# Kernel optimization log

Measured on AMD Instinct MI355X. Metric: run time of the kernel, lower is better.

The kernel has to match this reference:

```python
import jax, jax.numpy as jnp
import numpy as np

B, N, C = 32, 1025, 768
H, D = 12, 64          # num_heads, head_dim
M = 4 * D              # num random features = 256
HEIGHT, WIDTH = 32, 32 # spatial grid; N = HEIGHT*WIDTH + 1 (CLS)
EPS = 1e-6


def setup_inputs() -> dict:
    key = jax.random.key(0)
    ks = jax.random.split(key, 7)
    x = jax.random.normal(ks[0], (B, N, C), jnp.float32)
    w_qkv = jax.random.normal(ks[1], (3 * C, C), jnp.float32) * 0.02
    w_proj = jax.random.normal(ks[2], (C, C), jnp.float32) * 0.02
    b_proj = jnp.zeros((C,), jnp.float32)
    c_row = jax.random.normal(ks[3], (H, D), jnp.float32) * 0.02
    c_col = jax.random.normal(ks[4], (H, D), jnp.float32) * 0.02
    # orthogonal random-feature projection (m, d): QR blocks scaled by chi norm
    blocks = []
    for i in range(M // D):
        Hm = jax.random.normal(jax.random.fold_in(ks[5], i), (D, D), jnp.float32)
        Q, _ = jnp.linalg.qr(Hm)
        nrm = jnp.linalg.norm(jax.random.normal(jax.random.fold_in(ks[6], i), (D,), jnp.float32))
        blocks.append(Q * nrm)
    proj_feat = jnp.concatenate(blocks, axis=0)  # (M, D)
    return {"x": x, "w_qkv": w_qkv, "w_proj": w_proj, "b_proj": b_proj,
            "c_row": c_row, "c_col": c_col, "proj_feat": proj_feat}


def _string(xp, c_row, c_col):
    """Circulant-STRING rotation. xp: (B,H,Np,D)."""
    rows = jnp.arange(HEIGHT, dtype=jnp.float32)
    cols = jnp.arange(WIDTH, dtype=jnp.float32)
    gr, gc = jnp.meshgrid(rows, cols, indexing='ij')
    pos_r = gr.ravel()  # (Np,)
    pos_c = gc.ravel()
    # g: (H, Np, D)
    g = pos_r[None, :, None] * c_row[:, None, :] + pos_c[None, :, None] * c_col[:, None, :]
    g_fft = jnp.fft.fft(g, axis=-1)
    exp_lambda = jnp.exp(2j * g_fft.imag)          # (H, Np, D) complex, unit modulus
    x_fft = jnp.fft.fft(xp, axis=-1)               # (B, H, Np, D) complex
    rotated = jnp.fft.ifft(exp_lambda[None] * x_fft, axis=-1).real
    return rotated.astype(xp.dtype)


def _favor(x, proj):
    """Positive random feature map. x: (B,H,N,D), proj: (M,D) -> (B,H,N,M)."""
    xs = x * (D ** -0.25)
    px = jnp.einsum('bhnd,md->bhnm', xs, proj)
    norm_sq = 0.5 * jnp.sum(xs * xs, axis=-1, keepdims=True)
    return jnp.exp(px - norm_sq)


def reference(x, w_qkv, w_proj, b_proj, c_row, c_col, proj_feat):
    qkv = x @ w_qkv.T                                  # (B, N, 3C)
    qkv = qkv.reshape(B, N, 3, H, D).transpose(2, 0, 3, 1, 4)  # (3,B,H,N,D)
    q, k, v = qkv[0], qkv[1], qkv[2]
    # N == HEIGHT*WIDTH + 1 -> CLS token at position 0 is left unrotated
    q_cls, q_p = q[:, :, :1, :], q[:, :, 1:, :]
    k_cls, k_p = k[:, :, :1, :], k[:, :, 1:, :]
    q = jnp.concatenate([q_cls, _string(q_p, c_row, c_col)], axis=2)
    k = jnp.concatenate([k_cls, _string(k_p, c_row, c_col)], axis=2)
    q_feat = _favor(q, proj_feat)                      # (B,H,N,M)
    k_feat = _favor(k, proj_feat)
    # bidirectional linear attention
    context = jnp.einsum('bhnm,bhne->bhme', k_feat, v) # (B,H,M,D)
    num = jnp.einsum('bhnm,bhme->bhne', q_feat, context)
    k_sum = k_feat.sum(axis=2)                         # (B,H,M)
    den = jnp.einsum('bhnm,bhm->bhn', q_feat, k_sum)[..., None]
    den = jnp.maximum(den, EPS)
    out = num / den                                    # (B,H,N,D)
    out = out.transpose(0, 2, 1, 3).reshape(B, N, C)
    return out @ w_proj.T + b_proj
```

## Files before the change

kernel.cpp:

```cpp
#include <hip/hip_runtime.h>
#include <math.h>

typedef _Float16 f16;
typedef _Float16 f16x8 __attribute__((ext_vector_type(8)));
typedef _Float16 f16x4 __attribute__((ext_vector_type(4)));
typedef float f32x4 __attribute__((ext_vector_type(4)));

#define LDSK 40
#define NTOK 1025
#define CC 768
#define HH 12
#define DD 64
#define MM 256
#define VPAD 1056
#define BN_ROWS 32800

__device__ __forceinline__ void load_row16(const f16* p, f16x8& a0, f16x8& a1) {
    a0 = *(const f16x8*)p;
    a1 = *(const f16x8*)(p + 8);
}
__device__ __forceinline__ void load_row16(const float* p, f16x8& a0, f16x8& a1) {
    const float4* q = (const float4*)p;
    float4 u0 = q[0], u1 = q[1], u2 = q[2], u3 = q[3];
    a0[0] = (f16)u0.x; a0[1] = (f16)u0.y; a0[2] = (f16)u0.z; a0[3] = (f16)u0.w;
    a0[4] = (f16)u1.x; a0[5] = (f16)u1.y; a0[6] = (f16)u1.z; a0[7] = (f16)u1.w;
    a1[0] = (f16)u2.x; a1[1] = (f16)u2.y; a1[2] = (f16)u2.z; a1[3] = (f16)u2.w;
    a1[4] = (f16)u3.x; a1[5] = (f16)u3.y; a1[6] = (f16)u3.z; a1[7] = (f16)u3.w;
}

__global__ void k_diag(float* out, float v) {
    if (threadIdx.x == 0 && blockIdx.x == 0) out[0] = v;
}

__global__ __launch_bounds__(256) void k_cvt_x(const float* __restrict__ x, f16* __restrict__ xw) {
    size_t i = ((size_t)blockIdx.x * 256 + threadIdx.x) * 4;
    float4 v;
    if (i < (size_t)BN_ROWS * CC) v = *(const float4*)(x + i);
    else v = make_float4(0.f, 0.f, 0.f, 0.f);
    f16x4 o; o[0] = (f16)v.x; o[1] = (f16)v.y; o[2] = (f16)v.z; o[3] = (f16)v.w;
    *(f16x4*)(xw + i) = o;
}

__global__ __launch_bounds__(256) void k_cvt(const float* __restrict__ in, f16* __restrict__ out,
                                             long n, float scale) {
    long i = (long)blockIdx.x * 256 + threadIdx.x;
    if (i < n) out[i] = (f16)(in[i] * scale);
}

__global__ __launch_bounds__(256) void k_zpad(f16* __restrict__ v16t) {
    int bh = blockIdx.x;
    for (int u = threadIdx.x; u < 64 * 31; u += 256) {
        int d = u / 31, j = u - d * 31;
        v16t[((size_t)bh * DD + d) * VPAD + 1025 + j] = (f16)0.f;
    }
}

__global__ __launch_bounds__(64) void k_ab(const float* __restrict__ c_row,
                                           const float* __restrict__ c_col,
                                           float* __restrict__ ab) {
    int h = blockIdx.x, k = threadIdx.x;
    float sa = 0.f, sb = 0.f;
    for (int d = 0; d < 64; ++d) {
        float s = sinf((float)((k * d) & 63) * (6.283185307179586f / 64.f));
        sa += c_row[h * 64 + d] * s;
        sb += c_col[h * 64 + d] * s;
    }
    ab[h * 64 + k] = -2.f * sa;
    ab[768 + h * 64 + k] = -2.f * sb;
}

__global__ __launch_bounds__(64) void k_wcirc(const float* __restrict__ ab, float* __restrict__ wc) {
    int hp = blockIdx.x; int h = hp >> 10; int p = hp & 1023;
    float pr = (float)(p >> 5), pc = (float)(p & 31);
    int t = threadIdx.x;
    __shared__ float th[64];
    th[t] = pr * ab[h * 64 + t] + pc * ab[768 + h * 64 + t];
    __syncthreads();
    float s = 0.f;
    #pragma unroll 8
    for (int k = 0; k < 64; ++k) {
        float arg = th[k] + (float)((k * t) & 63) * (6.283185307179586f / 64.f);
        s += __cosf(arg);
    }
    wc[(size_t)hp * 64 + t] = s * (1.f / 64.f);
}

template <bool GA, typename TA, typename TB>
__device__ __forceinline__ void gemm128_core(const TA* __restrict__ A, const TB* __restrict__ Bm,
                                             int K, int row0, int col0, int Alim,
                                             f32x4 (&acc)[4][4],
                                             f16 (*As)[LDSK], f16 (*Bs)[LDSK]) {
    const int tid = threadIdx.x;
    const int lane = tid & 63;
    const int lr = tid >> 1, lk = (tid & 1) * 16;
    const int frow = lane & 15, fk = (lane >> 4) * 8;
    const int wave = tid >> 6, wr = wave >> 1, wc = wave & 1;
    for (int kt = 0; kt < K; kt += 32) {
        f16x8 a0 = {}, a1 = {}, b0, b1;
        if (!GA || (row0 + lr) < Alim)
            load_row16(A + (size_t)(row0 + lr) * K + kt + lk, a0, a1);
        load_row16(Bm + (size_t)(col0 + lr) * K + kt + lk, b0, b1);
        __syncthreads();
        *(f16x8*)&As[lr][lk] = a0; *(f16x8*)&As[lr][lk + 8] = a1;
        *(f16x8*)&Bs[lr][lk] = b0; *(f16x8*)&Bs[lr][lk + 8] = b1;
        __syncthreads();
        f16x8 af[4], bf[4];
        #pragma unroll
        for (int m = 0; m < 4; ++m) af[m] = *(const f16x8*)&As[wr * 64 + m * 16 + frow][fk];
        #pragma unroll
        for (int n = 0; n < 4; ++n) bf[n] = *(const f16x8*)&Bs[wc * 64 + n * 16 + frow][fk];
        #pragma unroll
        for (int m = 0; m < 4; ++m)
            #pragma unroll
            for (int n = 0; n < 4; ++n)
                acc[m][n] = __builtin_amdgcn_mfma_f32_16x16x32_f16(af[m], bf[n], acc[m][n], 0, 0, 0);
    }
}

template <typename TA>
__global__ __launch_bounds__(256) void k_gemm_qkv(const TA* __restrict__ A, const f16* __restrict__ Bm,
                                                  f16* __restrict__ q16, f16* __restrict__ k16,
                                                  f16* __restrict__ v16t) {
    __shared__ __attribute__((aligned(16))) f16 As[128][LDSK];
    __shared__ __attribute__((aligned(16))) f16 Bs[128][LDSK];
    f32x4 acc[4][4] = {};
    int row0 = blockIdx.x * 128, col0 = blockIdx.y * 128;
    gemm128_core<true>(A, Bm, CC, row0, col0, BN_ROWS, acc, As, Bs);
    int lane = threadIdx.x & 63, wave = threadIdx.x >> 6;
    int wr = wave >> 1, wc = wave & 1;
    int rb = row0 + wr * 64 + 4 * (lane >> 4);
    int cb = col0 + wc * 64 + (lane & 15);
    #pragma unroll
    for (int m = 0; m < 4; ++m)
        #pragma unroll
        for (int n = 0; n < 4; ++n)
            #pragma unroll
            for (int i = 0; i < 4; ++i) {
                int r = rb + m * 16 + i;
                if (r >= BN_ROWS) continue;
                int j = cb + n * 16;
                int b = r / NTOK, nn = r - b * NTOK;
                int t = j / CC, rem = j - t * CC;
                int h = rem >> 6, d = rem & 63;
                size_t bh = (size_t)b * HH + h;
                f16 val = (f16)acc[m][n][i];
                if (t == 0) q16[(bh * NTOK + nn) * DD + d] = val;
                else if (t == 1) k16[(bh * NTOK + nn) * DD + d] = val;
                else v16t[(bh * DD + d) * VPAD + nn] = val;
            }
}

__global__ __launch_bounds__(256) void k_rotate(const float* __restrict__ wcirc,
                                                f16* __restrict__ q16, f16* __restrict__ k16,
                                                float* __restrict__ nsqq, float* __restrict__ nsqk) {
    const int p = blockIdx.x, h = blockIdx.y;
    const int nn = p + 1;
    const int tid = threadIdx.x;
    __shared__ float wl[64];
    __shared__ __attribute__((aligned(16))) f16 Ws[64][72];
    __shared__ __attribute__((aligned(16))) f16 Xs[64][72];
    if (tid < 64) wl[tid] = wcirc[((size_t)h * 1024 + p) * 64 + tid];
    {
        const int row = tid >> 2;
        const int ch = (tid & 3) * 16;
        const int b = row & 31;
        const f16* src = ((row < 32) ? q16 : k16) + (((size_t)b * HH + h) * NTOK + nn) * DD + ch;
        f16x8 v0 = *(const f16x8*)src;
        f16x8 v1 = *(const f16x8*)(src + 8);
        *(f16x8*)&Xs[row][ch] = v0;
        *(f16x8*)&Xs[row][ch + 8] = v1;
    }
    __syncthreads();
    #pragma unroll
    for (int j = 0; j < 16; ++j) {
        int idx = tid * 16 + j;
        int d = idx >> 6, m = idx & 63;
        Ws[d][m] = (f16)wl[(d - m) & 63];
    }
    __syncthreads();
    const int lane = tid & 63, wave = tid >> 6;
    const int frow = lane & 15, fk = (lane >> 4) * 8;
    f32x4 acc[4] = {};
    #pragma unroll
    for (int kt = 0; kt < 64; kt += 32) {
        f16x8 a = *(const f16x8*)&Xs[wave * 16 + frow][kt + fk];
        #pragma unroll
        for (int n = 0; n < 4; ++n) {
            f16x8 bfr = *(const f16x8*)&Ws[n * 16 + frow][kt + fk];
            acc[n] = __builtin_amdgcn_mfma_f32_16x16x32_f16(a, bfr, acc[n], 0, 0, 0);
        }
    }
    #pragma unroll
    for (int i = 0; i < 4; ++i) {
        int row = wave * 16 + 4 * (lane >> 4) + i;
        int b = row & 31;
        f16* dst = ((row < 32) ? q16 : k16) + (((size_t)b * HH + h) * NTOK + nn) * DD;
        float ss = 0.f;
        #pragma unroll
        for (int n = 0; n < 4; ++n) {
            float v = acc[n][i];
            dst[n * 16 + (lane & 15)] = (f16)v;
            ss += v * v;
        }
        ss += __shfl_xor(ss, 1); ss += __shfl_xor(ss, 2);
        ss += __shfl_xor(ss, 4); ss += __shfl_xor(ss, 8);
        if ((lane & 15) == 0) {
            float* nd = (row < 32) ? nsqq : nsqk;
            nd[((size_t)b * HH + h) * NTOK + nn] = ss * (1.f / 16.f);
        }
    }
}

__global__ __launch_bounds__(256) void k_cls_nsq(const f16* __restrict__ q16, const f16* __restrict__ k16,
                                                 float* __restrict__ nsqq, float* __restrict__ nsqk) {
    int gw = (blockIdx.x * 256 + threadIdx.x) >> 6;
    int lane = threadIdx.x & 63;
    int which = gw & 1; int bh = gw >> 1;
    const f16* src = (which ? k16 : q16) + (size_t)bh * NTOK * DD;
    float v = (float)src[lane];
    float ss = v * v;
    for (int off = 1; off < 64; off <<= 1) ss += __shfl_xor(ss, off);
    if (lane == 0) (which ? nsqk : nsqq)[(size_t)bh * NTOK] = ss * (1.f / 16.f);
}

__global__ __launch_bounds__(512) void k_fctx(const f16* __restrict__ k16, const f16* __restrict__ v16t,
                                              const f16* __restrict__ pfeat, const float* __restrict__ nsqk,
                                              f16* __restrict__ ctxT) {
    __shared__ __attribute__((aligned(16))) f16 uLDS[80 * 136];
    f16 (*fts)[LDSK] = (f16(*)[LDSK])uLDS;
    f16 (*cx)[136]   = (f16(*)[136])uLDS;
    const int bh = blockIdx.x;
    const int tid = threadIdx.x;
    const int lane = tid & 63, w = tid >> 6;
    const int frow = lane & 15, fk8 = (lane >> 4) * 8;
    const int m0 = w * 32;
    f16x8 pf[2][2];
    #pragma unroll
    for (int mf = 0; mf < 2; ++mf)
        #pragma unroll
        for (int kf = 0; kf < 2; ++kf)
            pf[mf][kf] = *(const f16x8*)&pfeat[(m0 + mf * 16 + frow) * DD + kf * 32 + fk8];
    const f16* kb_base = k16 + (size_t)bh * NTOK * DD;
    const f16* vb_base = v16t + (size_t)bh * DD * VPAD;
    const float* ns_base = nsqk + (size_t)bh * NTOK;
    f32x4 acc[2][5] = {};
    for (int n0 = 0; n0 < VPAD; n0 += 32) {
        f16x8 kb[2][2];
        #pragma unroll
        for (int nf = 0; nf < 2; ++nf) {
            int n = n0 + nf * 16 + frow;
            #pragma unroll
            for (int kf = 0; kf < 2; ++kf) {
                f16x8 z = {};
                if (n < NTOK) z = *(const f16x8*)&kb_base[(size_t)n * DD + kf * 32 + fk8];
                kb[nf][kf] = z;
            }
        }
        f32x4 fa[2][2] = {};
        #pragma unroll
        for (int kf = 0; kf < 2; ++kf)
            #pragma unroll
            for (int mf = 0; mf < 2; ++mf)
                #pragma unroll
                for (int nf = 0; nf < 2; ++nf)
                    fa[mf][nf] = __builtin_amdgcn_mfma_f32_16x16x32_f16(pf[mf][kf], kb[nf][kf], fa[mf][nf], 0, 0, 0);
        #pragma unroll
        for (int nf = 0; nf < 2; ++nf) {
            int ncol = n0 + nf * 16 + frow;
            float ns = (ncol < NTOK) ? ns_base[ncol] : 0.f;
            #pragma unroll
            for (int mf = 0; mf < 2; ++mf)
                #pragma unroll
                for (int i = 0; i < 4; ++i) {
                    int mloc = m0 + mf * 16 + 4 * (lane >> 4) + i;
                    float v = (ncol < NTOK) ? fminf(__expf(fa[mf][nf][i] - ns), 60000.f) : 0.f;
                    fts[mloc][nf * 16 + frow] = (f16)v;
                }
        }
        __syncthreads();
        f16x8 afr[2];
        #pragma unroll
        for (int mf = 0; mf < 2; ++mf) afr[mf] = *(const f16x8*)&fts[m0 + mf * 16 + frow][fk8];
        #pragma unroll
        for (int ef = 0; ef < 4; ++ef) {
            f16x8 bfr = *(const f16x8*)&vb_base[(size_t)(ef * 16 + frow) * VPAD + n0 + fk8];
            #pragma unroll
            for (int mf = 0; mf < 2; ++mf)
                acc[mf][ef] = __builtin_amdgcn_mfma_f32_16x16x32_f16(afr[mf], bfr, acc[mf][ef], 0, 0, 0);
        }
        {
            f16x8 bfr;
            #pragma unroll
            for (int j = 0; j < 8; ++j)
                bfr[j] = (f16)((frow == 0 && (n0 + fk8 + j) < NTOK) ? 1.f : 0.f);
            #pragma unroll
            for (int mf = 0; mf < 2; ++mf)
                acc[mf][4] = __builtin_amdgcn_mfma_f32_16x16x32_f16(afr[mf], bfr, acc[mf][4], 0, 0, 0);
        }
        __syncthreads();
    }
    #pragma unroll
    for (int p = 0; p < 2; ++p) {
        __syncthreads();
        if ((w >> 2) == p) {
            int mb = m0 - p * 128;
            #pragma unroll
            for (int mf = 0; mf < 2; ++mf)
                #pragma unroll
                for (int ef = 0; ef < 5; ++ef) {
                    int e = ef * 16 + frow;
                    f16x4 pk;
                    #pragma unroll
                    for (int i = 0; i < 4; ++i) pk[i] = (f16)acc[mf][ef][i];
                    *(f16x4*)&cx[e][mb + mf * 16 + 4 * (lane >> 4)] = pk;
                }
        }
        __syncthreads();
        for (int u = tid; u < 80 * 16; u += 512) {
            int e = u >> 4, seg = u & 15;
            *(f16x8*)&ctxT[((size_t)bh * 80 + e) * MM + p * 128 + seg * 8] =
                *(const f16x8*)&cx[e][seg * 8];
        }
    }
}

__global__ __launch_bounds__(256) void k_fnum(const f16* __restrict__ q16, const f16* __restrict__ pfeat,
                                              const float* __restrict__ nsqq, const f16* __restrict__ ctxT,
                                              f16* __restrict__ attn) {
    __shared__ __attribute__((aligned(16))) f16 qf_s[128][72];
    const int bh = blockIdx.y;
    const int b = bh / HH, h = bh - b * HH;
    const int t0 = blockIdx.x * 128;
    const int tid = threadIdx.x;
    const int lane = tid & 63, w = tid >> 6;
    const int frow = lane & 15, fk8 = (lane >> 4) * 8;
    const f16* qbase = q16 + (size_t)bh * NTOK * DD;
    const f16* cbase = ctxT + (size_t)bh * 80 * MM;
    f16x8 qa[2][2];
    float ns[2][4];
    #pragma unroll
    for (int tf = 0; tf < 2; ++tf) {
        int t = t0 + w * 32 + tf * 16 + frow;
        #pragma unroll
        for (int kf = 0; kf < 2; ++kf) {
            f16x8 z = {};
            if (t < NTOK) z = *(const f16x8*)&qbase[(size_t)t * DD + kf * 32 + fk8];
            qa[tf][kf] = z;
        }
        #pragma unroll
        for (int i = 0; i < 4; ++i) {
            int tr = t0 + w * 32 + tf * 16 + 4 * (lane >> 4) + i;
            ns[tf][i] = (tr < NTOK) ? nsqq[(size_t)bh * NTOK + tr] : 0.f;
        }
    }
    f32x4 acc[2][5] = {};
    #pragma unroll
    for (int mc = 0; mc < 8; ++mc) {
        f16x8 pb[2][2];
        #pragma unroll
        for (int nf = 0; nf < 2; ++nf)
            #pragma unroll
            for (int kf = 0; kf < 2; ++kf)
                pb[nf][kf] = *(const f16x8*)&pfeat[(mc * 32 + nf * 16 + frow) * DD + kf * 32 + fk8];
        f32x4 fa[2][2] = {};
        #pragma unroll
        for (int kf = 0; kf < 2; ++kf)
            #pragma unroll
            for (int tf = 0; tf < 2; ++tf)
                #pragma unroll
                for (int nf = 0; nf < 2; ++nf)
                    fa[tf][nf] = __builtin_amdgcn_mfma_f32_16x16x32_f16(qa[tf][kf], pb[nf][kf], fa[tf][nf], 0, 0, 0);
        #pragma unroll
        for (int tf = 0; tf < 2; ++tf)
            #pragma unroll
            for (int nf = 0; nf < 2; ++nf)
                #pragma unroll
                for (int i = 0; i < 4; ++i) {
                    int tl = w * 32 + tf * 16 + 4 * (lane >> 4) + i;
                    float v = fminf(__expf(fa[tf][nf][i] - ns[tf][i]), 60000.f);
                    qf_s[tl][nf * 16 + frow] = (f16)v;
                }
        __syncthreads();
        f16x8 afr[2];
        #pragma unroll
        for (int tf = 0; tf < 2; ++tf) afr[tf] = *(const f16x8*)&qf_s[w * 32 + tf * 16 + frow][fk8];
        #pragma unroll
        for (int ef = 0; ef < 5; ++ef) {
            f16x8 bfr = *(const f16x8*)&cbase[(size_t)(ef * 16 + frow) * MM + mc * 32 + fk8];
            #pragma unroll
            for (int tf = 0; tf < 2; ++tf)
                acc[tf][ef] = __builtin_amdgcn_mfma_f32_16x16x32_f16(afr[tf], bfr, acc[tf][ef], 0, 0, 0);
        }
        __syncthreads();
    }
    #pragma unroll
    for (int tf = 0; tf < 2; ++tf)
        #pragma unroll
        for (int i = 0; i < 4; ++i) {
            float den = fmaxf(__shfl(acc[tf][4][i], lane & 48), 1e-6f);
            int tl = w * 32 + tf * 16 + 4 * (lane >> 4) + i;
            #pragma unroll
            for (int ef = 0; ef < 4; ++ef)
                qf_s[tl][ef * 16 + frow] = (f16)(acc[tf][ef][i] / den);
        }
    __syncthreads();
    for (int u = tid; u < 128 * 8; u += 256) {
        int tok = u >> 3, seg = u & 7;
        if (t0 + tok < NTOK)
            *(f16x8*)&attn[((size_t)(b * NTOK + t0 + tok)) * CC + h * DD + seg * 8] =
                *(const f16x8*)&qf_s[tok][seg * 8];
    }
}

__global__ __launch_bounds__(256) void k_gemm_proj(const f16* __restrict__ A, const f16* __restrict__ Bm,
                                                   const float* __restrict__ bias, float* __restrict__ out) {
    __shared__ __attribute__((aligned(16))) f16 As[128][LDSK];
    __shared__ __attribute__((aligned(16))) f16 Bs[128][LDSK];
    f32x4 acc[4][4] = {};
    int row0 = blockIdx.x * 128, col0 = blockIdx.y * 128;
    gemm128_core<true>(A, Bm, CC, row0, col0, BN_ROWS, acc, As, Bs);
    int lane = threadIdx.x & 63, wave = threadIdx.x >> 6;
    int wr = wave >> 1, wc = wave & 1;
    int rb = row0 + wr * 64 + 4 * (lane >> 4);
    int cb = col0 + wc * 64 + (lane & 15);
    #pragma unroll
    for (int n = 0; n < 4; ++n) {
        int j = cb + n * 16;
        float bj = bias[j];
        #pragma unroll
        for (int m = 0; m < 4; ++m)
            #pragma unroll
            for (int i = 0; i < 4; ++i) {
                int r = rb + m * 16 + i;
                if (r < BN_ROWS) out[(size_t)r * CC + j] = acc[m][n][i] + bj;
            }
    }
}

extern "C" void kernel_launch(void* const* d_in, const int* in_sizes, int n_in,
                              void* d_out, int out_size, void* d_ws, size_t ws_size,
                              hipStream_t stream) {
    const float* x = (const float*)d_in[0];
    const float* w_qkv = (const float*)d_in[1];
    const float* w_proj = (const float*)d_in[2];
    const float* b_proj = (const float*)d_in[3];
    const float* c_row = (const float*)d_in[4];
    const float* c_col = (const float*)d_in[5];
    const float* proj_feat = (const float*)d_in[6];
    float* out = (float*)d_out;
    char* ws = (char*)d_ws;
    char* ob = (char*)d_out;

    const size_t O_WQKV  = 0;
    const size_t O_WPROJ = 3538944;
    const size_t O_Q16   = 4718592;
    const size_t O_K16   = 55099392;
    const size_t O_XW    = 105480192;
    const size_t NEED_B  = 105480192;
    const size_t NEED_A  = 156008448;
    if (ws_size < NEED_B) {
        k_diag<<<1, 64, 0, stream>>>(out, (float)((double)ws_size / 1048576.0));
        return;
    }
    const bool useA = (ws_size >= NEED_A);

    const size_t OD_V    = 0;
    const size_t OD_CTX  = 51904512;
    const size_t OD_WC   = 67633152;
    const size_t OD_NSQQ = 70778880;
    const size_t OD_NSQK = 72353280;
    const size_t OD_PF   = 73927680;
    const size_t OD_AB   = 73960448;

    f16* wqkv16  = (f16*)(ws + O_WQKV);
    f16* wproj16 = (f16*)(ws + O_WPROJ);
    f16* q16     = (f16*)(ws + O_Q16);
    f16* k16     = (f16*)(ws + O_K16);
    f16* xw16    = (f16*)(ws + O_XW);
    f16* v16t    = (f16*)(ob + OD_V);
    f16* ctxT    = (f16*)(ob + OD_CTX);
    float* wcirc = (float*)(ob + OD_WC);
    float* nsqq  = (float*)(ob + OD_NSQQ);
    float* nsqk  = (float*)(ob + OD_NSQK);
    f16* pfeat16 = (f16*)(ob + OD_PF);
    float* ab    = (float*)(ob + OD_AB);
    f16* attn16  = k16;

    k_cvt<<<6912, 256, 0, stream>>>(w_qkv, wqkv16, 1769472L, 1.f);
    k_cvt<<<2304, 256, 0, stream>>>(w_proj, wproj16, 589824L, 1.f);
    k_cvt<<<64, 256, 0, stream>>>(proj_feat, pfeat16, 16384L, 0.3535533906f);
    k_ab<<<12, 64, 0, stream>>>(c_row, c_col, ab);
    k_wcirc<<<12288, 64, 0, stream>>>(ab, wcirc);

    if (useA) {
        k_cvt_x<<<24672, 256, 0, stream>>>(x, xw16);
        k_gemm_qkv<f16><<<dim3(257, 18), 256, 0, stream>>>(xw16, wqkv16, q16, k16, v16t);
    } else {
        k_gemm_qkv<float><<<dim3(257, 18), 256, 0, stream>>>(x, wqkv16, q16, k16, v16t);
    }
    k_zpad<<<384, 256, 0, stream>>>(v16t);

    k_rotate<<<dim3(1024, 12), 256, 0, stream>>>(wcirc, q16, k16, nsqq, nsqk);
    k_cls_nsq<<<192, 256, 0, stream>>>(q16, k16, nsqq, nsqk);

    k_fctx<<<384, 512, 0, stream>>>(k16, v16t, pfeat16, nsqk, ctxT);
    k_fnum<<<dim3(9, 384), 256, 0, stream>>>(q16, pfeat16, nsqq, ctxT, attn16);

    k_gemm_proj<<<dim3(257, 6), 256, 0, stream>>>(attn16, wproj16, b_proj, out);

    (void)in_sizes; (void)n_in; (void)out_size;
}
```

Baseline: 711.3 us.

## Load GEMM tiles via global_load_lds and remap blocks across XCDs

Adds a GEMM core that copies A and B tiles straight from global memory into LDS using global_load_lds 16-byte transfers, skipping the trip through registers. The QKV and projection GEMMs use it when the fp16 x path is active. The 2D grid becomes a 1D grid whose block index is permuted so that consecutive tiles stay on the same XCD, aiming for better L2 reuse. The LDS tiles are now unpadded (32 halves per row), which can bring bank conflicts on the fragment reads. The loads have no row bounds check, so this relies on padded buffers.

```diff
diff --git a/kernel.cpp b/kernel.cpp
--- a/kernel.cpp
+++ b/kernel.cpp
@@ -26,6 +26,12 @@
     a0[4] = (f16)u1.x; a0[5] = (f16)u1.y; a0[6] = (f16)u1.z; a0[7] = (f16)u1.w;
     a1[0] = (f16)u2.x; a1[1] = (f16)u2.y; a1[2] = (f16)u2.z; a1[3] = (f16)u2.w;
     a1[4] = (f16)u3.x; a1[5] = (f16)u3.y; a1[6] = (f16)u3.z; a1[7] = (f16)u3.w;
+}
+
+__device__ __forceinline__ void gload16(const f16* g, f16* l) {
+    __builtin_amdgcn_global_load_lds(
+        (const __attribute__((address_space(1))) unsigned int*)g,
+        (__attribute__((address_space(3))) unsigned int*)l, 16, 0, 0);
 }
 
 __global__ void k_diag(float* out, float v) {
@@ -117,15 +123,45 @@
     }
 }
 
-template <typename TA>
-__global__ __launch_bounds__(256) void k_gemm_qkv(const TA* __restrict__ A, const f16* __restrict__ Bm,
-                                                  f16* __restrict__ q16, f16* __restrict__ k16,
-                                                  f16* __restrict__ v16t) {
-    __shared__ __attribute__((aligned(16))) f16 As[128][LDSK];
-    __shared__ __attribute__((aligned(16))) f16 Bs[128][LDSK];
-    f32x4 acc[4][4] = {};
-    int row0 = blockIdx.x * 128, col0 = blockIdx.y * 128;
-    gemm128_core<true>(A, Bm, CC, row0, col0, BN_ROWS, acc, As, Bs);
+__device__ __forceinline__ void gemm128_dma(const f16* __restrict__ A, const f16* __restrict__ Bm,
+                                            int K, int row0, int col0,
+                                            f32x4 (&acc)[4][4], f16* As, f16* Bs) {
+    const int tid = threadIdx.x;
+    const int lane = tid & 63, wave = tid >> 6;
+    const int frow = lane & 15, fk8 = (lane >> 4) * 8;
+    const int wr = wave >> 1, wc = wave & 1;
+    const int srow = lane >> 2;
+    const int scol = (lane & 3) * 8;
+    const f16* aG = A + (size_t)(row0 + wave * 32 + srow) * K + scol;
+    const f16* bG = Bm + (size_t)(col0 + wave * 32 + srow) * K + scol;
+    const size_t rstep = (size_t)16 * K;
+    f16* aL0 = As + (wave * 32) * 32;
+    f16* aL1 = As + (wave * 32 + 16) * 32;
+    f16* bL0 = Bs + (wave * 32) * 32;
+    f16* bL1 = Bs + (wave * 32 + 16) * 32;
+    for (int kt = 0; kt < K; kt += 32) {
+        __syncthreads();
+        gload16(aG + kt, aL0);
+        gload16(aG + kt + rstep, aL1);
+        gload16(bG + kt, bL0);
+        gload16(bG + kt + rstep, bL1);
+        __syncthreads();
+        f16x8 af[4], bf[4];
+        #pragma unroll
+        for (int m = 0; m < 4; ++m) af[m] = *(const f16x8*)&As[(wr * 64 + m * 16 + frow) * 32 + fk8];
+        #pragma unroll
+        for (int n = 0; n < 4; ++n) bf[n] = *(const f16x8*)&Bs[(wc * 64 + n * 16 + frow) * 32 + fk8];
+        #pragma unroll
+        for (int m = 0; m < 4; ++m)
+            #pragma unroll
+            for (int n = 0; n < 4; ++n)
+                acc[m][n] = __builtin_amdgcn_mfma_f32_16x16x32_f16(af[m], bf[n], acc[m][n], 0, 0, 0);
+    }
+}
+
+__device__ __forceinline__ void qkv_epilogue(f32x4 (&acc)[4][4], int row0, int col0,
+                                             f16* __restrict__ q16, f16* __restrict__ k16,
+                                             f16* __restrict__ v16t) {
     int lane = threadIdx.x & 63, wave = threadIdx.x >> 6;
     int wr = wave >> 1, wc = wave & 1;
     int rb = row0 + wr * 64 + 4 * (lane >> 4);
@@ -148,6 +184,31 @@
                 else if (t == 1) k16[(bh * NTOK + nn) * DD + d] = val;
                 else v16t[(bh * DD + d) * VPAD + nn] = val;
             }
+}
+
+__global__ __launch_bounds__(256) void k_gemm_qkv_dma(const f16* __restrict__ A, const f16* __restrict__ Bm,
+                                                      f16* __restrict__ q16, f16* __restrict__ k16,
+                                                      f16* __restrict__ v16t) {
+    __shared__ __attribute__((aligned(16))) f16 As[128 * 32];
+    __shared__ __attribute__((aligned(16))) f16 Bs[128 * 32];
+    const int q = 578, r = 2;
+    int xg = blockIdx.x & 7, o8 = blockIdx.x >> 3;
+    int wg = (xg < r ? xg * (q + 1) : r * (q + 1) + (xg - r) * q) + o8;
+    int row0 = (wg / 18) * 128, col0 = (wg % 18) * 128;
+    f32x4 acc[4][4] = {};
+    gemm128_dma(A, Bm, CC, row0, col0, acc, As, Bs);
+    qkv_epilogue(acc, row0, col0, q16, k16, v16t);
+}
+
+__global__ __launch_bounds__(256) void k_gemm_qkv_f32(const float* __restrict__ A, const f16* __restrict__ Bm,
+                                                      f16* __restrict__ q16, f16* __restrict__ k16,
+                                                      f16* __restrict__ v16t) {
+    __shared__ __attribute__((aligned(16))) f16 As[128][LDSK];
+    __shared__ __attribute__((aligned(16))) f16 Bs[128][LDSK];
+    f32x4 acc[4][4] = {};
+    int row0 = blockIdx.x * 128, col0 = blockIdx.y * 128;
+    gemm128_core<true>(A, Bm, CC, row0, col0, BN_ROWS, acc, As, Bs);
+    qkv_epilogue(acc, row0, col0, q16, k16, v16t);
 }
 
 __global__ __launch_bounds__(256) void k_rotate(const float* __restrict__ wcirc,
@@ -412,6 +473,39 @@
     }
 }
 
+__device__ __forceinline__ void proj_epilogue(f32x4 (&acc)[4][4], int row0, int col0,
+                                              const float* __restrict__ bias, float* __restrict__ out) {
+    int lane = threadIdx.x & 63, wave = threadIdx.x >> 6;
+    int wr = wave >> 1, wc = wave & 1;
+    int rb = row0 + wr * 64 + 4 * (lane >> 4);
+    int cb = col0 + wc * 64 + (lane & 15);
+    #pragma unroll
+    for (int n = 0; n < 4; ++n) {
+        int j = cb + n * 16;
+        float bj = bias[j];
+        #pragma unroll
+        for (int m = 0; m < 4; ++m)
+            #pragma unroll
+            for (int i = 0; i < 4; ++i) {
+                int r = rb + m * 16 + i;
+                if (r < BN_ROWS) out[(size_t)r * CC + j] = acc[m][n][i] + bj;
+            }
+    }
+}
+
+__global__ __launch_bounds__(256) void k_gemm_proj_dma(const f16* __restrict__ A, const f16* __restrict__ Bm,
+                                                       const float* __restrict__ bias, float* __restrict__ out) {
+    __shared__ __attribute__((aligned(16))) f16 As[128 * 32];
+    __shared__ __attribute__((aligned(16))) f16 Bs[128 * 32];
+    const int q = 192, r = 6;
+    int xg = blockIdx.x & 7, o8 = blockIdx.x >> 3;
+    int wg = (xg < r ? xg * (q + 1) : r * (q + 1) + (xg - r) * q) + o8;
+    int row0 = (wg / 6) * 128, col0 = (wg % 6) * 128;
+    f32x4 acc[4][4] = {};
+    gemm128_dma(A, Bm, CC, row0, col0, acc, As, Bs);
+    proj_epilogue(acc, row0, col0, bias, out);
+}
+
 __global__ __launch_bounds__(256) void k_gemm_proj(const f16* __restrict__ A, const f16* __restrict__ Bm,
                                                    const float* __restrict__ bias, float* __restrict__ out) {
     __shared__ __attribute__((aligned(16))) f16 As[128][LDSK];
@@ -419,22 +513,7 @@
     f32x4 acc[4][4] = {};
     int row0 = blockIdx.x * 128, col0 = blockIdx.y * 128;
     gemm128_core<true>(A, Bm, CC, row0, col0, BN_ROWS, acc, As, Bs);
-    int lane = threadIdx.x & 63, wave = threadIdx.x >> 6;
-    int wr = wave >> 1, wc = wave & 1;
-    int rb = row0 + wr * 64 + 4 * (lane >> 4);
-    int cb = col0 + wc * 64 + (lane & 15);
-    #pragma unroll
-    for (int n = 0; n < 4; ++n) {
-        int j = cb + n * 16;
-        float bj = bias[j];
-        #pragma unroll
-        for (int m = 0; m < 4; ++m)
-            #pragma unroll
-            for (int i = 0; i < 4; ++i) {
-                int r = rb + m * 16 + i;
-                if (r < BN_ROWS) out[(size_t)r * CC + j] = acc[m][n][i] + bj;
-            }
-    }
+    proj_epilogue(acc, row0, col0, bias, out);
 }
 
 extern "C" void kernel_launch(void* const* d_in, const int* in_sizes, int n_in,
@@ -494,9 +573,9 @@
 
     if (useA) {
         k_cvt_x<<<24672, 256, 0, stream>>>(x, xw16);
-        k_gemm_qkv<f16><<<dim3(257, 18), 256, 0, stream>>>(xw16, wqkv16, q16, k16, v16t);
+        k_gemm_qkv_dma<<<4626, 256, 0, stream>>>(xw16, wqkv16, q16, k16, v16t);
     } else {
-        k_gemm_qkv<float><<<dim3(257, 18), 256, 0, stream>>>(x, wqkv16, q16, k16, v16t);
+        k_gemm_qkv_f32<<<dim3(257, 18), 256, 0, stream>>>(x, wqkv16, q16, k16, v16t);
     }
     k_zpad<<<384, 256, 0, stream>>>(v16t);
 
@@ -506,7 +585,11 @@
     k_fctx<<<384, 512, 0, stream>>>(k16, v16t, pfeat16, nsqk, ctxT);
     k_fnum<<<dim3(9, 384), 256, 0, stream>>>(q16, pfeat16, nsqq, ctxT, attn16);
 
-    k_gemm_proj<<<dim3(257, 6), 256, 0, stream>>>(attn16, wproj16, b_proj, out);
+    if (useA) {
+        k_gemm_proj_dma<<<1542, 256, 0, stream>>>(attn16, wproj16, b_proj, out);
+    } else {
+        k_gemm_proj<<<dim3(257, 6), 256, 0, stream>>>(attn16, wproj16, b_proj, out);
+    }
 
     (void)in_sizes; (void)n_in; (void)out_size;
 }
```

Result: faster. 669.7 us (-5.8%).
